# Kernel optimization log

Hardware: AMD Instinct MI355X
Metric: run time of the kernel (lower is better)

Reference implementation:

```python
import jax, jax.numpy as jnp
import numpy as np

N_NODE = 100000
EMB = 100
BATCH = 512
SEQ = 50
LAYERS = 2
NNZ = 1000000
BETA = 0.01


def setup_inputs() -> dict:
    key = jax.random.key(0)
    ks = jax.random.split(key, 16)
    stdv = 1.0 / np.sqrt(EMB)
    u = lambda k, shp: jax.random.uniform(k, shp, jnp.float32, -stdv, stdv)
    emb_weight = u(ks[0], (N_NODE, EMB))
    pos_weight = u(ks[1], (200, EMB))
    w_1 = u(ks[2], (2 * EMB, EMB))
    w_2 = u(ks[3], (EMB, 1))
    glu1_w = u(ks[4], (EMB, EMB))
    glu1_b = u(ks[5], (EMB,))
    glu2_w = u(ks[6], (EMB, EMB))
    # sparse hypergraph adjacency in COO form
    adj_rows = jax.random.randint(ks[7], (NNZ,), 0, N_NODE)
    adj_cols = jax.random.randint(ks[8], (NNZ,), 0, N_NODE)
    adj_vals = jax.random.uniform(ks[9], (NNZ,), jnp.float32, 0.0, 0.1)
    session_item = jax.random.randint(ks[10], (BATCH, SEQ), 0, N_NODE + 1)
    reversed_sess_item = jax.random.randint(ks[11], (BATCH, SEQ), 0, N_NODE + 1)
    session_len = jnp.ones((BATCH, 1), jnp.float32)
    mask = jnp.ones((BATCH, SEQ), jnp.float32)
    D = jax.random.uniform(ks[12], (BATCH, BATCH), jnp.float32, 0.0, 0.01)
    A = jax.random.uniform(ks[13], (BATCH, BATCH), jnp.float32, 0.0, 0.01)
    # fixed permutations standing in for torch.randperm in SSL
    perm_rows = jax.random.permutation(ks[14], BATCH)
    perm_cols = jax.random.permutation(ks[15], EMB)
    return {
        'session_item': session_item, 'session_len': session_len, 'D': D, 'A': A,
        'reversed_sess_item': reversed_sess_item, 'mask': mask,
        'emb_weight': emb_weight, 'pos_weight': pos_weight, 'w_1': w_1, 'w_2': w_2,
        'glu1_w': glu1_w, 'glu1_b': glu1_b, 'glu2_w': glu2_w,
        'adj_rows': adj_rows, 'adj_cols': adj_cols, 'adj_vals': adj_vals,
        'perm_rows': perm_rows, 'perm_cols': perm_cols,
    }


def reference(session_item, session_len, D, A, reversed_sess_item, mask,
              emb_weight, pos_weight, w_1, w_2, glu1_w, glu1_b, glu2_w,
              adj_rows, adj_cols, adj_vals, perm_rows, perm_cols):
    # ---- HyperConv: layers of sparse mm, summed over layer outputs ----
    h = emb_weight
    item_hg = h
    for _ in range(LAYERS):
        h = jax.ops.segment_sum(adj_vals[:, None] * h[adj_cols], adj_rows,
                                num_segments=N_NODE)
        item_hg = item_hg + h

    # ---- generate_sess_emb (gather + attention gate) ----
    pad_hg = jnp.concatenate([jnp.zeros((1, EMB), item_hg.dtype), item_hg], 0)
    seq_h = pad_hg[reversed_sess_item]                       # [B, L, d]
    hs = jnp.sum(seq_h, 1) / session_len                     # [B, d]
    pos = jnp.broadcast_to(pos_weight[:SEQ], (BATCH, SEQ, EMB))
    nh = jnp.tanh(jnp.concatenate([pos, seq_h], -1) @ w_1)   # [B, L, d]
    nh = jax.nn.sigmoid(nh @ glu1_w.T + glu1_b + (hs @ glu2_w.T)[:, None, :])
    att = (nh @ w_2) * mask[..., None]                       # [B, L, 1]
    sess_hg = jnp.sum(att * seq_h, 1)                        # [B, d]

    # ---- LineConv (line-graph propagation on raw embedding) ----
    pad0 = jnp.concatenate([jnp.zeros((1, EMB), emb_weight.dtype), emb_weight], 0)
    s = jnp.sum(pad0[session_item], 1) / session_len          # [B, d]
    sess_lg = s
    DA = D @ A
    for _ in range(LAYERS):
        s = DA @ s
        sess_lg = sess_lg + s

    # ---- SSL contrastive loss (fixed permutations replace randperm) ----
    pos_s = jnp.sum(sess_hg * sess_lg, 1)
    corrupt = sess_hg[perm_rows][:, perm_cols]
    neg1 = jnp.sum(sess_lg * corrupt, 1)
    con = jnp.sum(-jnp.log(1e-8 + jax.nn.sigmoid(pos_s))
                  - jnp.log(1e-8 + (1.0 - jax.nn.sigmoid(neg1))))

    # use_HG=True -> sess_emb is the hypergraph session embedding
    return item_hg, sess_hg, BETA * con
```

## Files before the change

### kernel.cpp

```cpp
#include <hip/hip_runtime.h>
#include <math.h>

#define N_NODE 100000
#define EMB    100
#define BATCH  512
#define SEQ    50
#define NNZ    1000000

#define SCAN_CHUNK 1024
#define SCAN_NB ((N_NODE + SCAN_CHUNK - 1) / SCAN_CHUNK)

static __device__ __forceinline__ float bf2f(unsigned short u) {
  union { unsigned int i; float f; } v; v.i = ((unsigned int)u) << 16; return v.f;
}
static __device__ __forceinline__ unsigned short f2bf(float f) {
  union { float f; unsigned int i; } v; v.f = f;
  unsigned int i = v.i;
  return (unsigned short)((i + 0x7fffu + ((i >> 16) & 1u)) >> 16);
}
static __device__ __forceinline__ float lo2f(unsigned int u) {
  union { unsigned int i; float f; } v; v.i = u << 16; return v.f;
}
static __device__ __forceinline__ float hi2f(unsigned int u) {
  union { unsigned int i; float f; } v; v.i = u & 0xffff0000u; return v.f;
}

__global__ void hist_kernel(const int* __restrict__ rows, int* __restrict__ counts) {
  int i = blockIdx.x * blockDim.x + threadIdx.x;
  if (i < NNZ) atomicAdd(&counts[rows[i]], 1);
}

__global__ void scan_partial_kernel(const int* __restrict__ counts, int* __restrict__ partial) {
  __shared__ int red[256];
  int b = blockIdx.x, t = threadIdx.x;
  int base = b * SCAN_CHUNK;
  int s = 0;
  #pragma unroll
  for (int k = 0; k < SCAN_CHUNK; k += 256) {
    int idx = base + k + t;
    if (idx < N_NODE) s += counts[idx];
  }
  red[t] = s;
  __syncthreads();
  for (int off = 128; off; off >>= 1) {
    if (t < off) red[t] += red[t + off];
    __syncthreads();
  }
  if (t == 0) partial[b] = red[0];
}

__global__ void scan_top_kernel(int* __restrict__ partial, int* __restrict__ row_ptr) {
  __shared__ int s[128];
  int t = threadIdx.x;
  int v = (t < SCAN_NB) ? partial[t] : 0;
  s[t] = v;
  __syncthreads();
  for (int off = 1; off < 128; off <<= 1) {
    int u = (t >= off) ? s[t - off] : 0;
    __syncthreads();
    s[t] += u;
    __syncthreads();
  }
  if (t < SCAN_NB) partial[t] = (t == 0) ? 0 : s[t - 1];
  if (t == 127) row_ptr[N_NODE] = s[127];
}

__global__ void scan_final_kernel(const int* __restrict__ partial,
                                  int* __restrict__ counts_cursor,
                                  int* __restrict__ row_ptr) {
  __shared__ int s[256];
  int b = blockIdx.x, t = threadIdx.x;
  int base = b * SCAN_CHUNK + t * 4;
  int c[4];
  #pragma unroll
  for (int k = 0; k < 4; ++k) {
    int idx = base + k;
    c[k] = (idx < N_NODE) ? counts_cursor[idx] : 0;
  }
  int local = c[0] + c[1] + c[2] + c[3];
  s[t] = local;
  __syncthreads();
  for (int off = 1; off < 256; off <<= 1) {
    int u = (t >= off) ? s[t - off] : 0;
    __syncthreads();
    s[t] += u;
    __syncthreads();
  }
  int prefix = partial[b] + ((t == 0) ? 0 : s[t - 1]);
  #pragma unroll
  for (int k = 0; k < 4; ++k) {
    int idx = base + k;
    if (idx < N_NODE) {
      row_ptr[idx] = prefix;
      counts_cursor[idx] = prefix;
      prefix += c[k];
    }
  }
}

__global__ void scatterA_kernel(const int* __restrict__ rows, const int* __restrict__ cols,
                                const float* __restrict__ vals, int* __restrict__ cursor,
                                int* __restrict__ cols_s, float* __restrict__ vals_s) {
  int i = blockIdx.x * blockDim.x + threadIdx.x;
  if (i >= NNZ) return;
  int p = atomicAdd(&cursor[rows[i]], 1);
  cols_s[p] = cols[i];
  vals_s[p] = vals[i];
}

__global__ void scatterB_kernel(const int* __restrict__ rows, const int* __restrict__ cols,
                                const float* __restrict__ vals, int* __restrict__ cursor,
                                unsigned short* __restrict__ colHi, unsigned char* __restrict__ colLo) {
  int i = blockIdx.x * blockDim.x + threadIdx.x;
  if (i >= NNZ) return;
  int p = atomicAdd(&cursor[rows[i]], 1);
  int c = cols[i];
  int q = (int)rintf(vals[i] * 1270.f);
  q = q < 0 ? 0 : (q > 127 ? 127 : q);
  colHi[p] = (unsigned short)(c >> 1);
  colLo[p] = (unsigned char)(((c & 1) << 7) | q);
}

__global__ void spmmA_kernel(const int* __restrict__ rp, const int* __restrict__ cols,
                             const float* __restrict__ vals,
                             const float2* __restrict__ gsrc, const float2* __restrict__ base,
                             float2* __restrict__ dst) {
  int w = (blockIdx.x * blockDim.x + threadIdx.x) >> 6;
  int lane = threadIdx.x & 63;
  if (w >= N_NODE || lane >= 50) return;
  int s = __builtin_amdgcn_readfirstlane(rp[w]);
  int e = __builtin_amdgcn_readfirstlane(rp[w + 1]);
  float ax[8], ay[8];
  #pragma unroll
  for (int k = 0; k < 8; ++k) { ax[k] = 0.f; ay[k] = 0.f; }
  for (int j = s; j < e; j += 8) {
    int   cc[8];
    float vv[8];
    #pragma unroll
    for (int k = 0; k < 8; ++k) {
      int jj = j + k;
      int jc = jj < e ? jj : e - 1;
      cc[k] = cols[jc];
      float v = vals[jc];
      vv[k] = (jj < e) ? v : 0.f;
    }
    float2 uu[8];
    #pragma unroll
    for (int k = 0; k < 8; ++k) uu[k] = gsrc[cc[k] * 50 + lane];
    #pragma unroll
    for (int k = 0; k < 8; ++k) { ax[k] += vv[k] * uu[k].x; ay[k] += vv[k] * uu[k].y; }
  }
  float sx = ((ax[0] + ax[1]) + (ax[2] + ax[3])) + ((ax[4] + ax[5]) + (ax[6] + ax[7]));
  float sy = ((ay[0] + ay[1]) + (ay[2] + ay[3])) + ((ay[4] + ay[5]) + (ay[6] + ay[7]));
  float2 ev = base[w * 50 + lane];
  dst[w * 50 + lane] = make_float2(ev.x + sx, ev.y + sy);
}

__global__ void spmmB_kernel(const int* __restrict__ rp, const unsigned short* __restrict__ colHi,
                             const unsigned char* __restrict__ colLo,
                             const float2* __restrict__ gsrc, const float2* __restrict__ base,
                             float2* __restrict__ dst) {
  int w = (blockIdx.x * blockDim.x + threadIdx.x) >> 6;
  int lane = threadIdx.x & 63;
  if (w >= N_NODE || lane >= 50) return;
  int s = __builtin_amdgcn_readfirstlane(rp[w]);
  int e = __builtin_amdgcn_readfirstlane(rp[w + 1]);
  float ax[8], ay[8];
  #pragma unroll
  for (int k = 0; k < 8; ++k) { ax[k] = 0.f; ay[k] = 0.f; }
  for (int j = s; j < e; j += 8) {
    int   cc[8];
    float vv[8];
    #pragma unroll
    for (int k = 0; k < 8; ++k) {
      int jj = j + k;
      int jc = jj < e ? jj : e - 1;
      int hi = colHi[jc], lo = colLo[jc];
      cc[k] = (hi << 1) | (lo >> 7);
      float v = (float)(lo & 0x7f) * (1.f / 1270.f);
      vv[k] = (jj < e) ? v : 0.f;
    }
    float2 uu[8];
    #pragma unroll
    for (int k = 0; k < 8; ++k) uu[k] = gsrc[cc[k] * 50 + lane];
    #pragma unroll
    for (int k = 0; k < 8; ++k) { ax[k] += vv[k] * uu[k].x; ay[k] += vv[k] * uu[k].y; }
  }
  float sx = ((ax[0] + ax[1]) + (ax[2] + ax[3])) + ((ax[4] + ax[5]) + (ax[6] + ax[7]));
  float sy = ((ay[0] + ay[1]) + (ay[2] + ay[3])) + ((ay[4] + ay[5]) + (ay[6] + ay[7]));
  float2 ev = base[w * 50 + lane];
  dst[w * 50 + lane] = make_float2(ev.x + sx, ev.y + sy);
}

__global__ void posw_kernel(const float* __restrict__ pos_w, const float* __restrict__ w1,
                            float* __restrict__ posW) {
  __shared__ float sp[EMB];
  int l = blockIdx.x, e = threadIdx.x;
  if (e < EMB) sp[e] = pos_w[l * EMB + e];
  __syncthreads();
  if (e < EMB) {
    float a = 0.f;
    for (int k = 0; k < EMB; ++k) a += sp[k] * w1[k * EMB + e];
    posW[l * EMB + e] = a;
  }
}

__global__ __launch_bounds__(512, 4) void sess_kernel(
    const int* __restrict__ rsi, const int* __restrict__ si,
    const float* __restrict__ item_hg,
    const float* __restrict__ emb, const float* __restrict__ slen,
    const float* __restrict__ posW, const float* __restrict__ w1,
    const float* __restrict__ glu1w, const float* __restrict__ glu1b,
    const float* __restrict__ glu2w, const float* __restrict__ w2,
    const float* __restrict__ maskp,
    float* __restrict__ X, float* __restrict__ Z,
    float* __restrict__ out_sess) {
  __shared__ __align__(16) float seq[SEQ * EMB];
  __shared__ unsigned int w1p[50 * EMB];
  __shared__ unsigned int g1p[50 * EMB];
  __shared__ float hsL[EMB];
  __shared__ __align__(16) float nhL[4][EMB];
  __shared__ float hsP[4][EMB];
  __shared__ float s0P[4][EMB];
  __shared__ float hsgP[4][EMB];
  __shared__ float accP[4][EMB];
  __shared__ float redg[4][2];
  int b = blockIdx.x, t = threadIdx.x;
  int g = t >> 7;
  int e = t & 127;
  bool act = e < EMB;

  for (int i = t; i < 50 * EMB; i += 512) {
    int kp = i / EMB, e2 = i % EMB;
    unsigned int b0 = f2bf(w1[EMB * EMB + (2 * kp) * EMB + e2]);
    unsigned int b1 = f2bf(w1[EMB * EMB + (2 * kp + 1) * EMB + e2]);
    w1p[i] = b0 | (b1 << 16);
    unsigned int c0 = f2bf(glu1w[e2 * EMB + 2 * kp]);
    unsigned int c1 = f2bf(glu1w[e2 * EMB + 2 * kp + 1]);
    g1p[i] = c0 | (c1 << 16);
  }

  float inv = 1.f / slen[b];

  float hsacc = 0.f, s0acc = 0.f;
  if (act) {
    for (int l = g; l < SEQ; l += 4) {
      int i1 = rsi[b * SEQ + l];
      float sv_ = (i1 > 0) ? item_hg[(i1 - 1) * EMB + e] : 0.f;
      seq[l * EMB + e] = sv_;
      hsacc += sv_;
      int i0 = si[b * SEQ + l];
      if (i0 > 0) s0acc += emb[(i0 - 1) * EMB + e];
    }
    hsP[g][e] = hsacc;
    s0P[g][e] = s0acc;
  }
  __syncthreads();
  if (act && g == 0) {
    float hv = (hsP[0][e] + hsP[1][e] + hsP[2][e] + hsP[3][e]) * inv;
    float sv = (s0P[0][e] + s0P[1][e] + s0P[2][e] + s0P[3][e]) * inv;
    hsL[e] = hv;
    X[b * EMB + e] = sv;
    Z[b * EMB + e] = sv;
  }
  __syncthreads();

  if (act) {
    float a = 0.f;
    int k0 = g * 25;
    for (int k = k0; k < k0 + 25; ++k) a += hsL[k] * glu2w[e * EMB + k];
    hsgP[g][e] = a;
  }
  __syncthreads();
  float hsgv = 0.f, w2v = 0.f;
  if (act) {
    hsgv = glu1b[e] + hsgP[0][e] + hsgP[1][e] + hsgP[2][e] + hsgP[3][e];
    w2v = w2[e];
  }

  float acc = 0.f;
  for (int it = 0; it < (SEQ + 3) / 4; ++it) {
    int l = it * 4 + g;
    bool lv = l < SEQ;
    __syncthreads();
    if (act && lv) {
      const float4* sq4 = (const float4*)&seq[l * EMB];
      float a0 = 0.f, a1 = 0.f, a2 = 0.f, a3 = 0.f;
      #pragma unroll
      for (int i = 0; i < 25; ++i) {
        float4 sv = sq4[i];
        unsigned int p0 = w1p[(2 * i) * EMB + e];
        unsigned int p1 = w1p[(2 * i + 1) * EMB + e];
        a0 += sv.x * lo2f(p0);
        a1 += sv.y * hi2f(p0);
        a2 += sv.z * lo2f(p1);
        a3 += sv.w * hi2f(p1);
      }
      float nh = posW[l * EMB + e] + ((a0 + a1) + (a2 + a3));
      nhL[g][e] = tanhf(nh);
    }
    __syncthreads();
    float p = 0.f;
    if (act && lv) {
      const float4* nq4 = (const float4*)nhL[g];
      float a0 = hsgv, a1 = 0.f, a2 = 0.f, a3 = 0.f;
      #pragma unroll
      for (int i = 0; i < 25; ++i) {
        float4 nv = nq4[i];
        unsigned int p0 = g1p[(2 * i) * EMB + e];
        unsigned int p1 = g1p[(2 * i + 1) * EMB + e];
        a0 += nv.x * lo2f(p0);
        a1 += nv.y * hi2f(p0);
        a2 += nv.z * lo2f(p1);
        a3 += nv.w * hi2f(p1);
      }
      float a = (a0 + a1) + (a2 + a3);
      float gs = 1.f / (1.f + __expf(-a));
      p = gs * w2v;
    }
    for (int off = 32; off; off >>= 1) p += __shfl_down(p, off, 64);
    if ((t & 63) == 0) redg[g][(t >> 6) & 1] = p;
    __syncthreads();
    if (act && lv) {
      float att = (redg[g][0] + redg[g][1]) * maskp[b * SEQ + l];
      acc += att * seq[l * EMB + e];
    }
  }
  if (act) accP[g][e] = acc;
  __syncthreads();
  if (act && g == 0)
    out_sess[b * EMB + e] = accP[0][e] + accP[1][e] + accP[2][e] + accP[3][e];
}

__global__ void mv_kernel(const float* __restrict__ M, const float* __restrict__ x,
                          float* __restrict__ y, float* __restrict__ Zacc) {
  __shared__ float Ms[BATCH];
  int b = blockIdx.x, t = threadIdx.x;
  for (int i = t; i < BATCH; i += 128) Ms[i] = M[b * BATCH + i];
  __syncthreads();
  if (t < EMB) {
    float a = 0.f;
    for (int k = 0; k < BATCH; ++k) a += Ms[k] * x[k * EMB + t];
    y[b * EMB + t] = a;
    if (Zacc) Zacc[b * EMB + t] += a;
  }
}

__global__ void ssl_kernel(const float* __restrict__ Z, const float* __restrict__ hg,
                           const int* __restrict__ pr, const int* __restrict__ pc,
                           float* __restrict__ loss) {
  __shared__ float r1[128], r2[128];
  int b = blockIdx.x, t = threadIdx.x;
  float p1 = 0.f, p2 = 0.f;
  if (t < EMB) {
    float lg = Z[b * EMB + t];
    p1 = lg * hg[b * EMB + t];
    p2 = lg * hg[pr[b] * EMB + pc[t]];
  }
  r1[t] = p1; r2[t] = p2;
  __syncthreads();
  for (int off = 64; off; off >>= 1) {
    if (t < off) { r1[t] += r1[t + off]; r2[t] += r2[t + off]; }
    __syncthreads();
  }
  if (t == 0) {
    float sp = 1.f / (1.f + expf(-r1[0]));
    float sn = 1.f / (1.f + expf(-r2[0]));
    atomicAdd(loss, -logf(1e-8f + sp) - logf(1e-8f + (1.f - sn)));
  }
}

__global__ void loss_write_kernel(const float* __restrict__ loss, float* __restrict__ out) {
  out[0] = 0.01f * loss[0];
}

extern "C" void kernel_launch(void* const* d_in, const int* in_sizes, int n_in,
                              void* d_out, int out_size, void* d_ws, size_t ws_size,
                              hipStream_t stream) {
  const int*   session_item = (const int*)d_in[0];
  const float* slen   = (const float*)d_in[1];
  const float* D      = (const float*)d_in[2];
  const float* A      = (const float*)d_in[3];
  const int*   rsi    = (const int*)d_in[4];
  const float* mask   = (const float*)d_in[5];
  const float* emb    = (const float*)d_in[6];
  const float* posw   = (const float*)d_in[7];
  const float* w1     = (const float*)d_in[8];
  const float* w2     = (const float*)d_in[9];
  const float* glu1w  = (const float*)d_in[10];
  const float* glu1b  = (const float*)d_in[11];
  const float* glu2w  = (const float*)d_in[12];
  const int*   adj_rows = (const int*)d_in[13];
  const int*   adj_cols = (const int*)d_in[14];
  const float* adj_vals = (const float*)d_in[15];
  const int*   pr     = (const int*)d_in[16];
  const int*   pc     = (const int*)d_in[17];

  float* out_item = (float*)d_out;
  float* out_sess = out_item + (size_t)N_NODE * EMB;
  float* out_loss = out_sess + (size_t)BATCH * EMB;
  float2* out2    = (float2*)d_out;
  const float2* emb2 = (const float2*)emb;

  char* ws = (char*)d_ws;
  size_t off = 0;
  auto alloc = [&](size_t bytes) -> void* {
    void* p = ws + off;
    off = (off + bytes + 255) & ~(size_t)255;
    return p;
  };

  if (ws_size >= 9800000) {
    int*   counts  = (int*)alloc((size_t)N_NODE * 4);
    int*   row_ptr = (int*)alloc((size_t)(N_NODE + 1) * 4);
    int*   partial = (int*)alloc((size_t)SCAN_NB * 4);
    int*   cols_s  = (int*)alloc((size_t)NNZ * 4);
    float* vals_s  = (float*)alloc((size_t)NNZ * 4);
    float* posW    = (float*)alloc((size_t)SEQ * EMB * 4);
    float* X       = (float*)alloc((size_t)BATCH * EMB * 4);
    float* Y       = (float*)alloc((size_t)BATCH * EMB * 4);
    float* Z       = (float*)alloc((size_t)BATCH * EMB * 4);
    float* loss    = (float*)alloc(256);

    hipMemsetAsync(counts, 0, (size_t)N_NODE * 4, stream);
    hipMemsetAsync(loss, 0, 4, stream);

    hist_kernel<<<(NNZ + 255) / 256, 256, 0, stream>>>(adj_rows, counts);
    scan_partial_kernel<<<SCAN_NB, 256, 0, stream>>>(counts, partial);
    scan_top_kernel<<<1, 128, 0, stream>>>(partial, row_ptr);
    scan_final_kernel<<<SCAN_NB, 256, 0, stream>>>(partial, counts, row_ptr);
    scatterA_kernel<<<(NNZ + 255) / 256, 256, 0, stream>>>(adj_rows, adj_cols, adj_vals,
                                                           counts, cols_s, vals_s);
    spmmA_kernel<<<N_NODE / 4, 256, 0, stream>>>(row_ptr, cols_s, vals_s, emb2, emb2, out2);
    spmmA_kernel<<<N_NODE / 4, 256, 0, stream>>>(row_ptr, cols_s, vals_s, out2, emb2, out2);

    posw_kernel<<<SEQ, 128, 0, stream>>>(posw, w1, posW);
    sess_kernel<<<BATCH, 512, 0, stream>>>(rsi, session_item, out_item, emb, slen, posW,
                                           w1, glu1w, glu1b, glu2w, w2, mask,
                                           X, Z, out_sess);
    mv_kernel<<<BATCH, 128, 0, stream>>>(A, X, Y, (float*)nullptr);
    mv_kernel<<<BATCH, 128, 0, stream>>>(D, Y, X, Z);
    mv_kernel<<<BATCH, 128, 0, stream>>>(A, X, Y, (float*)nullptr);
    mv_kernel<<<BATCH, 128, 0, stream>>>(D, Y, X, Z);
    ssl_kernel<<<BATCH, 128, 0, stream>>>(Z, out_sess, pr, pc, loss);
    loss_write_kernel<<<1, 1, 0, stream>>>(loss, out_loss);
  } else {
    unsigned short* colHi  = (unsigned short*)alloc((size_t)NNZ * 2);
    unsigned char*  colLo  = (unsigned char*)alloc((size_t)NNZ);
    int*            row_ptr = (int*)alloc((size_t)(N_NODE + 1) * 4);
    int*            partial = (int*)alloc((size_t)SCAN_NB * 4);
    size_t u0 = off;
    int*   counts = (int*)alloc((size_t)N_NODE * 4);
    off = u0;
    float* posW = (float*)alloc((size_t)SEQ * EMB * 4);
    float* X    = (float*)alloc((size_t)BATCH * EMB * 4);
    float* Y    = (float*)alloc((size_t)BATCH * EMB * 4);
    float* Z    = (float*)alloc((size_t)BATCH * EMB * 4);
    float* loss = (float*)alloc(256);

    hipMemsetAsync(counts, 0, (size_t)N_NODE * 4, stream);

    hist_kernel<<<(NNZ + 255) / 256, 256, 0, stream>>>(adj_rows, counts);
    scan_partial_kernel<<<SCAN_NB, 256, 0, stream>>>(counts, partial);
    scan_top_kernel<<<1, 128, 0, stream>>>(partial, row_ptr);
    scan_final_kernel<<<SCAN_NB, 256, 0, stream>>>(partial, counts, row_ptr);
    scatterB_kernel<<<(NNZ + 255) / 256, 256, 0, stream>>>(adj_rows, adj_cols, adj_vals,
                                                           counts, colHi, colLo);
    spmmB_kernel<<<N_NODE / 4, 256, 0, stream>>>(row_ptr, colHi, colLo, emb2, emb2, out2);
    spmmB_kernel<<<N_NODE / 4, 256, 0, stream>>>(row_ptr, colHi, colLo, out2, emb2, out2);

    hipMemsetAsync(loss, 0, 4, stream);
    posw_kernel<<<SEQ, 128, 0, stream>>>(posw, w1, posW);
    sess_kernel<<<BATCH, 512, 0, stream>>>(rsi, session_item, out_item, emb, slen, posW,
                                           w1, glu1w, glu1b, glu2w, w2, mask,
                                           X, Z, out_sess);
    mv_kernel<<<BATCH, 128, 0, stream>>>(A, X, Y, (float*)nullptr);
    mv_kernel<<<BATCH, 128, 0, stream>>>(D, Y, X, Z);
    mv_kernel<<<BATCH, 128, 0, stream>>>(A, X, Y, (float*)nullptr);
    mv_kernel<<<BATCH, 128, 0, stream>>>(D, Y, X, Z);
    ssl_kernel<<<BATCH, 128, 0, stream>>>(Z, out_sess, pr, pc, loss);
    loss_write_kernel<<<1, 1, 0, stream>>>(loss, out_loss);
  }
}
```

Measured before the change: 573.0 us.

## Pack CSR col+quantized value into one word, restructure session kernel per-wavefront

The scatter now writes each nonzero's column index and a 15-bit quantized value into a single 32-bit word, and the SpMM decodes it. This halves the index/value traffic and shrinks the workspace needed for the fast path. The session kernel moves from 4 groups of 128 threads to 8 wavefronts, each handling 2 embedding lanes. That removes the per-step block barriers and shared-memory attention reductions in favour of wave-level shuffles. The loss is also accumulated directly into the output, pre-scaled, which drops a kernel launch; quantizing the adjacency values adds accuracy risk.

```diff
diff --git a/kernel.cpp b/kernel.cpp
--- a/kernel.cpp
+++ b/kernel.cpp
@@ -100,12 +100,13 @@
 
 __global__ void scatterA_kernel(const int* __restrict__ rows, const int* __restrict__ cols,
                                 const float* __restrict__ vals, int* __restrict__ cursor,
-                                int* __restrict__ cols_s, float* __restrict__ vals_s) {
+                                unsigned int* __restrict__ cv) {
   int i = blockIdx.x * blockDim.x + threadIdx.x;
   if (i >= NNZ) return;
   int p = atomicAdd(&cursor[rows[i]], 1);
-  cols_s[p] = cols[i];
-  vals_s[p] = vals[i];
+  int q = (int)rintf(vals[i] * 327670.f);
+  q = q < 0 ? 0 : (q > 32767 ? 32767 : q);
+  cv[p] = ((unsigned int)cols[i] << 15) | (unsigned int)q;
 }
 
 __global__ void scatterB_kernel(const int* __restrict__ rows, const int* __restrict__ cols,
@@ -121,8 +122,7 @@
   colLo[p] = (unsigned char)(((c & 1) << 7) | q);
 }
 
-__global__ void spmmA_kernel(const int* __restrict__ rp, const int* __restrict__ cols,
-                             const float* __restrict__ vals,
+__global__ void spmmA_kernel(const int* __restrict__ rp, const unsigned int* __restrict__ cv,
                              const float2* __restrict__ gsrc, const float2* __restrict__ base,
                              float2* __restrict__ dst) {
   int w = (blockIdx.x * blockDim.x + threadIdx.x) >> 6;
@@ -140,8 +140,9 @@
     for (int k = 0; k < 8; ++k) {
       int jj = j + k;
       int jc = jj < e ? jj : e - 1;
-      cc[k] = cols[jc];
-      float v = vals[jc];
+      unsigned int u = cv[jc];
+      cc[k] = (int)(u >> 15);
+      float v = (float)(u & 0x7fffu) * (1.f / 327670.f);
       vv[k] = (jj < e) ? v : 0.f;
     }
     float2 uu[8];
@@ -219,16 +220,18 @@
   __shared__ unsigned int w1p[50 * EMB];
   __shared__ unsigned int g1p[50 * EMB];
   __shared__ float hsL[EMB];
-  __shared__ __align__(16) float nhL[4][EMB];
-  __shared__ float hsP[4][EMB];
-  __shared__ float s0P[4][EMB];
-  __shared__ float hsgP[4][EMB];
-  __shared__ float accP[4][EMB];
-  __shared__ float redg[4][2];
+  __shared__ float hsgL[EMB];
+  __shared__ __align__(16) float nhL[8][EMB];
+  __shared__ float hsP[8][EMB];
+  __shared__ float s0P[8][EMB];
+  __shared__ float accP[8][EMB];
   int b = blockIdx.x, t = threadIdx.x;
-  int g = t >> 7;
-  int e = t & 127;
-  bool act = e < EMB;
+  int w = t >> 6;
+  int lane = t & 63;
+  int e0 = lane;
+  int e1 = lane + 64;
+  bool has1 = e1 < EMB;
+  int e1x = has1 ? e1 : e0;
 
   for (int i = t; i < 50 * EMB; i += 512) {
     int kp = i / EMB, e2 = i % EMB;
@@ -242,94 +245,116 @@
 
   float inv = 1.f / slen[b];
 
-  float hsacc = 0.f, s0acc = 0.f;
-  if (act) {
-    for (int l = g; l < SEQ; l += 4) {
-      int i1 = rsi[b * SEQ + l];
-      float sv_ = (i1 > 0) ? item_hg[(i1 - 1) * EMB + e] : 0.f;
-      seq[l * EMB + e] = sv_;
-      hsacc += sv_;
-      int i0 = si[b * SEQ + l];
-      if (i0 > 0) s0acc += emb[(i0 - 1) * EMB + e];
-    }
-    hsP[g][e] = hsacc;
-    s0P[g][e] = s0acc;
-  }
-  __syncthreads();
-  if (act && g == 0) {
-    float hv = (hsP[0][e] + hsP[1][e] + hsP[2][e] + hsP[3][e]) * inv;
-    float sv = (s0P[0][e] + s0P[1][e] + s0P[2][e] + s0P[3][e]) * inv;
-    hsL[e] = hv;
-    X[b * EMB + e] = sv;
-    Z[b * EMB + e] = sv;
-  }
-  __syncthreads();
-
-  if (act) {
-    float a = 0.f;
-    int k0 = g * 25;
-    for (int k = k0; k < k0 + 25; ++k) a += hsL[k] * glu2w[e * EMB + k];
-    hsgP[g][e] = a;
-  }
-  __syncthreads();
-  float hsgv = 0.f, w2v = 0.f;
-  if (act) {
-    hsgv = glu1b[e] + hsgP[0][e] + hsgP[1][e] + hsgP[2][e] + hsgP[3][e];
-    w2v = w2[e];
-  }
-
-  float acc = 0.f;
-  for (int it = 0; it < (SEQ + 3) / 4; ++it) {
-    int l = it * 4 + g;
-    bool lv = l < SEQ;
-    __syncthreads();
-    if (act && lv) {
-      const float4* sq4 = (const float4*)&seq[l * EMB];
-      float a0 = 0.f, a1 = 0.f, a2 = 0.f, a3 = 0.f;
-      #pragma unroll
-      for (int i = 0; i < 25; ++i) {
-        float4 sv = sq4[i];
-        unsigned int p0 = w1p[(2 * i) * EMB + e];
-        unsigned int p1 = w1p[(2 * i + 1) * EMB + e];
-        a0 += sv.x * lo2f(p0);
-        a1 += sv.y * hi2f(p0);
-        a2 += sv.z * lo2f(p1);
-        a3 += sv.w * hi2f(p1);
-      }
-      float nh = posW[l * EMB + e] + ((a0 + a1) + (a2 + a3));
-      nhL[g][e] = tanhf(nh);
-    }
-    __syncthreads();
-    float p = 0.f;
-    if (act && lv) {
-      const float4* nq4 = (const float4*)nhL[g];
-      float a0 = hsgv, a1 = 0.f, a2 = 0.f, a3 = 0.f;
-      #pragma unroll
-      for (int i = 0; i < 25; ++i) {
-        float4 nv = nq4[i];
-        unsigned int p0 = g1p[(2 * i) * EMB + e];
-        unsigned int p1 = g1p[(2 * i + 1) * EMB + e];
-        a0 += nv.x * lo2f(p0);
-        a1 += nv.y * hi2f(p0);
-        a2 += nv.z * lo2f(p1);
-        a3 += nv.w * hi2f(p1);
-      }
-      float a = (a0 + a1) + (a2 + a3);
-      float gs = 1.f / (1.f + __expf(-a));
-      p = gs * w2v;
-    }
-    for (int off = 32; off; off >>= 1) p += __shfl_down(p, off, 64);
-    if ((t & 63) == 0) redg[g][(t >> 6) & 1] = p;
-    __syncthreads();
-    if (act && lv) {
-      float att = (redg[g][0] + redg[g][1]) * maskp[b * SEQ + l];
-      acc += att * seq[l * EMB + e];
-    }
-  }
-  if (act) accP[g][e] = acc;
-  __syncthreads();
-  if (act && g == 0)
-    out_sess[b * EMB + e] = accP[0][e] + accP[1][e] + accP[2][e] + accP[3][e];
+  float hs0 = 0.f, hs1 = 0.f, s00 = 0.f, s01 = 0.f;
+  for (int l = w; l < SEQ; l += 8) {
+    int i1 = rsi[b * SEQ + l];
+    float v0 = (i1 > 0) ? item_hg[(i1 - 1) * EMB + e0] : 0.f;
+    seq[l * EMB + e0] = v0;
+    hs0 += v0;
+    if (has1) {
+      float v1 = (i1 > 0) ? item_hg[(i1 - 1) * EMB + e1] : 0.f;
+      seq[l * EMB + e1] = v1;
+      hs1 += v1;
+    }
+    int i0 = si[b * SEQ + l];
+    if (i0 > 0) {
+      s00 += emb[(i0 - 1) * EMB + e0];
+      if (has1) s01 += emb[(i0 - 1) * EMB + e1];
+    }
+  }
+  hsP[w][e0] = hs0;
+  s0P[w][e0] = s00;
+  if (has1) { hsP[w][e1] = hs1; s0P[w][e1] = s01; }
+  __syncthreads();
+
+  if (t < EMB) {
+    float hv = 0.f, sv = 0.f;
+    #pragma unroll
+    for (int k = 0; k < 8; ++k) { hv += hsP[k][t]; sv += s0P[k][t]; }
+    hv *= inv; sv *= inv;
+    hsL[t] = hv;
+    X[b * EMB + t] = sv;
+    Z[b * EMB + t] = sv;
+  }
+  __syncthreads();
+
+  if (t < EMB) {
+    const float* gw = &glu2w[t * EMB];
+    float a0 = 0.f, a1 = 0.f, a2 = 0.f, a3 = 0.f;
+    for (int k = 0; k < EMB; k += 4) {
+      a0 += hsL[k]     * gw[k];
+      a1 += hsL[k + 1] * gw[k + 1];
+      a2 += hsL[k + 2] * gw[k + 2];
+      a3 += hsL[k + 3] * gw[k + 3];
+    }
+    hsgL[t] = glu1b[t] + ((a0 + a1) + (a2 + a3));
+  }
+  __syncthreads();
+
+  float hsg0 = hsgL[e0];
+  float hsg1 = hsgL[e1x];
+  float w2v0 = w2[e0];
+  float w2v1 = has1 ? w2[e1] : 0.f;
+
+  float acc0 = 0.f, acc1 = 0.f;
+  for (int l = w; l < SEQ; l += 8) {
+    const float4* sq4 = (const float4*)&seq[l * EMB];
+    float a0 = 0.f, a1 = 0.f, a2 = 0.f, a3 = 0.f;
+    float b0 = 0.f, b1 = 0.f, b2 = 0.f, b3 = 0.f;
+    #pragma unroll
+    for (int i = 0; i < 25; ++i) {
+      float4 sv = sq4[i];
+      unsigned int p0 = w1p[(2 * i) * EMB + e0];
+      unsigned int p1 = w1p[(2 * i + 1) * EMB + e0];
+      a0 += sv.x * lo2f(p0); a1 += sv.y * hi2f(p0);
+      a2 += sv.z * lo2f(p1); a3 += sv.w * hi2f(p1);
+      unsigned int q0 = w1p[(2 * i) * EMB + e1x];
+      unsigned int q1 = w1p[(2 * i + 1) * EMB + e1x];
+      b0 += sv.x * lo2f(q0); b1 += sv.y * hi2f(q0);
+      b2 += sv.z * lo2f(q1); b3 += sv.w * hi2f(q1);
+    }
+    nhL[w][e0] = tanhf(posW[l * EMB + e0] + ((a0 + a1) + (a2 + a3)));
+    if (has1)
+      nhL[w][e1] = tanhf(posW[l * EMB + e1] + ((b0 + b1) + (b2 + b3)));
+
+    const float4* nq4 = (const float4*)&nhL[w][0];
+    a0 = hsg0; a1 = 0.f; a2 = 0.f; a3 = 0.f;
+    b0 = hsg1; b1 = 0.f; b2 = 0.f; b3 = 0.f;
+    #pragma unroll
+    for (int i = 0; i < 25; ++i) {
+      float4 nv = nq4[i];
+      unsigned int p0 = g1p[(2 * i) * EMB + e0];
+      unsigned int p1 = g1p[(2 * i + 1) * EMB + e0];
+      a0 += nv.x * lo2f(p0); a1 += nv.y * hi2f(p0);
+      a2 += nv.z * lo2f(p1); a3 += nv.w * hi2f(p1);
+      unsigned int q0 = g1p[(2 * i) * EMB + e1x];
+      unsigned int q1 = g1p[(2 * i + 1) * EMB + e1x];
+      b0 += nv.x * lo2f(q0); b1 += nv.y * hi2f(q0);
+      b2 += nv.z * lo2f(q1); b3 += nv.w * hi2f(q1);
+    }
+    float sA = (a0 + a1) + (a2 + a3);
+    float g0 = 1.f / (1.f + __expf(-sA));
+    float p = g0 * w2v0;
+    if (has1) {
+      float sB = (b0 + b1) + (b2 + b3);
+      float g1 = 1.f / (1.f + __expf(-sB));
+      p += g1 * w2v1;
+    }
+    #pragma unroll
+    for (int off = 32; off; off >>= 1) p += __shfl_xor(p, off, 64);
+    float att = p * maskp[b * SEQ + l];
+    acc0 += att * seq[l * EMB + e0];
+    if (has1) acc1 += att * seq[l * EMB + e1];
+  }
+  accP[w][e0] = acc0;
+  if (has1) accP[w][e1] = acc1;
+  __syncthreads();
+  if (t < EMB) {
+    float s = 0.f;
+    #pragma unroll
+    for (int k = 0; k < 8; ++k) s += accP[k][t];
+    out_sess[b * EMB + t] = s;
+  }
 }
 
 __global__ void mv_kernel(const float* __restrict__ M, const float* __restrict__ x,
@@ -348,7 +373,7 @@
 
 __global__ void ssl_kernel(const float* __restrict__ Z, const float* __restrict__ hg,
                            const int* __restrict__ pr, const int* __restrict__ pc,
-                           float* __restrict__ loss) {
+                           float* __restrict__ loss_out) {
   __shared__ float r1[128], r2[128];
   int b = blockIdx.x, t = threadIdx.x;
   float p1 = 0.f, p2 = 0.f;
@@ -366,12 +391,8 @@
   if (t == 0) {
     float sp = 1.f / (1.f + expf(-r1[0]));
     float sn = 1.f / (1.f + expf(-r2[0]));
-    atomicAdd(loss, -logf(1e-8f + sp) - logf(1e-8f + (1.f - sn)));
-  }
-}
-
-__global__ void loss_write_kernel(const float* __restrict__ loss, float* __restrict__ out) {
-  out[0] = 0.01f * loss[0];
+    atomicAdd(loss_out, 0.01f * (-logf(1e-8f + sp) - logf(1e-8f + (1.f - sn))));
+  }
 }
 
 extern "C" void kernel_launch(void* const* d_in, const int* in_sizes, int n_in,
@@ -410,29 +431,28 @@
     return p;
   };
 
-  if (ws_size >= 9800000) {
-    int*   counts  = (int*)alloc((size_t)N_NODE * 4);
-    int*   row_ptr = (int*)alloc((size_t)(N_NODE + 1) * 4);
-    int*   partial = (int*)alloc((size_t)SCAN_NB * 4);
-    int*   cols_s  = (int*)alloc((size_t)NNZ * 4);
-    float* vals_s  = (float*)alloc((size_t)NNZ * 4);
-    float* posW    = (float*)alloc((size_t)SEQ * EMB * 4);
-    float* X       = (float*)alloc((size_t)BATCH * EMB * 4);
-    float* Y       = (float*)alloc((size_t)BATCH * EMB * 4);
-    float* Z       = (float*)alloc((size_t)BATCH * EMB * 4);
-    float* loss    = (float*)alloc(256);
+  hipMemsetAsync(out_loss, 0, 4, stream);
+
+  if (ws_size >= 5500000) {
+    int*          counts  = (int*)alloc((size_t)N_NODE * 4);
+    int*          row_ptr = (int*)alloc((size_t)(N_NODE + 1) * 4);
+    int*          partial = (int*)alloc((size_t)SCAN_NB * 4);
+    unsigned int* cv      = (unsigned int*)alloc((size_t)NNZ * 4);
+    float* posW = (float*)alloc((size_t)SEQ * EMB * 4);
+    float* X    = (float*)alloc((size_t)BATCH * EMB * 4);
+    float* Y    = (float*)alloc((size_t)BATCH * EMB * 4);
+    float* Z    = (float*)alloc((size_t)BATCH * EMB * 4);
 
     hipMemsetAsync(counts, 0, (size_t)N_NODE * 4, stream);
-    hipMemsetAsync(loss, 0, 4, stream);
 
     hist_kernel<<<(NNZ + 255) / 256, 256, 0, stream>>>(adj_rows, counts);
     scan_partial_kernel<<<SCAN_NB, 256, 0, stream>>>(counts, partial);
     scan_top_kernel<<<1, 128, 0, stream>>>(partial, row_ptr);
     scan_final_kernel<<<SCAN_NB, 256, 0, stream>>>(partial, counts, row_ptr);
     scatterA_kernel<<<(NNZ + 255) / 256, 256, 0, stream>>>(adj_rows, adj_cols, adj_vals,
-                                                           counts, cols_s, vals_s);
-    spmmA_kernel<<<N_NODE / 4, 256, 0, stream>>>(row_ptr, cols_s, vals_s, emb2, emb2, out2);
-    spmmA_kernel<<<N_NODE / 4, 256, 0, stream>>>(row_ptr, cols_s, vals_s, out2, emb2, out2);
+                                                           counts, cv);
+    spmmA_kernel<<<N_NODE / 4, 256, 0, stream>>>(row_ptr, cv, emb2, emb2, out2);
+    spmmA_kernel<<<N_NODE / 4, 256, 0, stream>>>(row_ptr, cv, out2, emb2, out2);
 
     posw_kernel<<<SEQ, 128, 0, stream>>>(posw, w1, posW);
     sess_kernel<<<BATCH, 512, 0, stream>>>(rsi, session_item, out_item, emb, slen, posW,
@@ -442,8 +462,7 @@
     mv_kernel<<<BATCH, 128, 0, stream>>>(D, Y, X, Z);
     mv_kernel<<<BATCH, 128, 0, stream>>>(A, X, Y, (float*)nullptr);
     mv_kernel<<<BATCH, 128, 0, stream>>>(D, Y, X, Z);
-    ssl_kernel<<<BATCH, 128, 0, stream>>>(Z, out_sess, pr, pc, loss);
-    loss_write_kernel<<<1, 1, 0, stream>>>(loss, out_loss);
+    ssl_kernel<<<BATCH, 128, 0, stream>>>(Z, out_sess, pr, pc, out_loss);
   } else {
     unsigned short* colHi  = (unsigned short*)alloc((size_t)NNZ * 2);
     unsigned char*  colLo  = (unsigned char*)alloc((size_t)NNZ);
@@ -456,7 +475,6 @@
     float* X    = (float*)alloc((size_t)BATCH * EMB * 4);
     float* Y    = (float*)alloc((size_t)BATCH * EMB * 4);
     float* Z    = (float*)alloc((size_t)BATCH * EMB * 4);
-    float* loss = (float*)alloc(256);
 
     hipMemsetAsync(counts, 0, (size_t)N_NODE * 4, stream);
 
@@ -469,7 +487,6 @@
     spmmB_kernel<<<N_NODE / 4, 256, 0, stream>>>(row_ptr, colHi, colLo, emb2, emb2, out2);
     spmmB_kernel<<<N_NODE / 4, 256, 0, stream>>>(row_ptr, colHi, colLo, out2, emb2, out2);
 
-    hipMemsetAsync(loss, 0, 4, stream);
     posw_kernel<<<SEQ, 128, 0, stream>>>(posw, w1, posW);
     sess_kernel<<<BATCH, 512, 0, stream>>>(rsi, session_item, out_item, emb, slen, posW,
                                            w1, glu1w, glu1b, glu2w, w2, mask,
@@ -478,7 +495,6 @@
     mv_kernel<<<BATCH, 128, 0, stream>>>(D, Y, X, Z);
     mv_kernel<<<BATCH, 128, 0, stream>>>(A, X, Y, (float*)nullptr);
     mv_kernel<<<BATCH, 128, 0, stream>>>(D, Y, X, Z);
-    ssl_kernel<<<BATCH, 128, 0, stream>>>(Z, out_sess, pr, pc, loss);
-    loss_write_kernel<<<1, 1, 0, stream>>>(loss, out_loss);
-  }
-}
+    ssl_kernel<<<BATCH, 128, 0, stream>>>(Z, out_sess, pr, pc, out_loss);
+  }
+}
```

After: 1.159 ms. 2.02x slower.
